# Kernel optimization log

Hardware: AMD Instinct MI355X
Metric: run time of the kernel (lower is better)

Reference implementation:

```python
import jax, jax.numpy as jnp
import numpy as np
import math

N_EMBED = 1024
N_HEAD = 16
HS = N_EMBED // N_HEAD

def setup_inputs() -> dict:
    key = jax.random.key(0)
    ks = jax.random.split(key, 5)
    s = 1.0 / math.sqrt(N_EMBED)
    x = jax.random.normal(ks[0], (2, 2048, N_EMBED), dtype=jnp.float32)
    W_qkv = jax.random.uniform(ks[1], (N_EMBED, 3 * N_EMBED), dtype=jnp.float32, minval=-s, maxval=s)
    b_qkv = jax.random.uniform(ks[2], (3 * N_EMBED,), dtype=jnp.float32, minval=-s, maxval=s)
    W_out = jax.random.uniform(ks[3], (N_EMBED, N_EMBED), dtype=jnp.float32, minval=-s, maxval=s)
    b_out = jax.random.uniform(ks[4], (N_EMBED,), dtype=jnp.float32, minval=-s, maxval=s)
    return {"x": x, "W_qkv": W_qkv, "b_qkv": b_qkv, "W_out": W_out, "b_out": b_out}

def reference(x, W_qkv, b_qkv, W_out, b_out):
    bs, seq_len, dim = x.shape
    qkv = x @ W_qkv + b_qkv                      # [b, s, 3*d]
    q, k, v = jnp.split(qkv, 3, axis=-1)
    def heads(t):
        return t.reshape(bs, seq_len, N_HEAD, HS).transpose(0, 2, 1, 3)  # [b, h, s, hs]
    q, k, v = heads(q), heads(k), heads(v)
    scale = 1.0 / math.sqrt(HS)
    attn = jnp.einsum('bhqd,bhkd->bhqk', q, k) * scale  # [b, h, s, s]
    causal = jnp.tril(jnp.ones((seq_len, seq_len), dtype=bool))
    attn = jnp.where(causal, attn, -jnp.inf)
    attn = jax.nn.softmax(attn, axis=-1)
    o = jnp.einsum('bhqk,bhkd->bhqd', attn, v)   # [b, h, s, hs]
    o = o.transpose(0, 2, 1, 3).reshape(bs, seq_len, dim)
    return o @ W_out + b_out
```

## Files before the change

### kernel.cpp

```cpp
#include <hip/hip_runtime.h>
#include <hip/hip_bf16.h>
#include <stdint.h>

typedef __attribute__((ext_vector_type(4))) float f32x4;
typedef __attribute__((ext_vector_type(8))) short s16x8;
typedef __attribute__((ext_vector_type(4))) short s16x4;

#define B_   2
#define S_   2048
#define D_   1024
#define H_   16
#define HS_  64
#define TOK  (B_*S_)
#define BH_  (B_*H_)

__device__ __forceinline__ short f2bf(float f){
  union { float f; uint32_t u; } v; v.f = f;
  uint32_t u = v.u;
  u += 0x7fffu + ((u >> 16) & 1u);
  return (short)(u >> 16);
}

__device__ __forceinline__ uint32_t cvt_pk_bf16(float lo, float hi){
  uint32_t r;
  asm("v_cvt_pk_bf16_f32 %0, %1, %2" : "=v"(r) : "v"(lo), "v"(hi));
  return r;
}

__device__ __forceinline__ void gload_lds16(const void* g, void* l){
  __builtin_amdgcn_global_load_lds((const __attribute__((address_space(1))) void*)g,
                                   (__attribute__((address_space(3))) void*)l, 16, 0, 0);
}

__global__ void k_cvt(const float* __restrict__ src, short* __restrict__ dst, int n4){
  int i = blockIdx.x * blockDim.x + threadIdx.x;
  if (i < n4){
    float4 v = reinterpret_cast<const float4*>(src)[i];
    s16x4 o;
    o.x = f2bf(v.x); o.y = f2bf(v.y); o.z = f2bf(v.z); o.w = f2bf(v.w);
    reinterpret_cast<s16x4*>(dst)[i] = o;
  }
}

__global__ void k_tconv(const float* __restrict__ src, short* __restrict__ dst, int K, int N){
  __shared__ short tile[32][33];
  const int n0 = blockIdx.x * 32, k0 = blockIdx.y * 32;
  const int c = threadIdx.x & 31, r8 = threadIdx.x >> 5;
  #pragma unroll
  for (int j = 0; j < 4; j++){
    int k = r8 + j * 8;
    tile[c][k] = f2bf(src[(size_t)(k0 + k) * N + n0 + c]);
  }
  __syncthreads();
  #pragma unroll
  for (int j = 0; j < 4; j++){
    int nl = r8 + j * 8;
    dst[(size_t)(n0 + nl) * K + k0 + c] = tile[nl][c];
  }
}

__global__ __launch_bounds__(256, 2) void k_gemm_qkv(
    const short* __restrict__ A, const short* __restrict__ Bt,
    const float* __restrict__ bias, short* __restrict__ Qb)
{
  __shared__ short Al[128 * 32];
  __shared__ short Bl[128 * 32];
  const int tid = threadIdx.x;
  const int lane = tid & 63, wave = tid >> 6;
  const int m0 = blockIdx.x * 128, n0 = blockIdx.y * 128;
  const int wm = (wave >> 1) * 64, wn = (wave & 1) * 64;
  const int c = lane & 15, g = lane >> 4;

  f32x4 acc[4][4];
  #pragma unroll
  for (int i = 0; i < 4; i++)
    #pragma unroll
    for (int j = 0; j < 4; j++) acc[i][j] = (f32x4){0.f, 0.f, 0.f, 0.f};

  const short* Asrc = A + (size_t)m0 * 1024;
  const short* Bsrc = Bt + (size_t)n0 * 1024;

  for (int kt = 0; kt < 1024; kt += 32){
    __syncthreads();
    #pragma unroll
    for (int j = 0; j < 2; j++){
      int gc = (wave * 2 + j) * 64 + lane;
      int row = gc >> 2, c8 = gc & 3;
      gload_lds16(Asrc + (size_t)row * 1024 + kt + c8 * 8, Al + (size_t)(wave * 2 + j) * 512);
      gload_lds16(Bsrc + (size_t)row * 1024 + kt + c8 * 8, Bl + (size_t)(wave * 2 + j) * 512);
    }
    __syncthreads();

    s16x8 af[4], bq[4];
    #pragma unroll
    for (int t = 0; t < 4; t++){
      af[t] = *(const s16x8*)&Al[(wm + t * 16 + c) * 32 + g * 8];
      bq[t] = *(const s16x8*)&Bl[(wn + t * 16 + c) * 32 + g * 8];
    }
    #pragma unroll
    for (int mt = 0; mt < 4; mt++)
      #pragma unroll
      for (int nt = 0; nt < 4; nt++)
        acc[mt][nt] = __builtin_amdgcn_mfma_f32_16x16x32_bf16(af[mt], bq[nt], acc[mt][nt], 0, 0, 0);
  }

  const size_t QSZ = (size_t)BH_ * S_ * HS_;
  #pragma unroll
  for (int mt = 0; mt < 4; mt++){
    #pragma unroll
    for (int nt = 0; nt < 4; nt++){
      int n = n0 + wn + nt * 16 + c;
      float bv = bias[n];
      int sel = n >> 10, hn = (n >> 6) & 15, d = n & 63;
      #pragma unroll
      for (int r = 0; r < 4; r++){
        int token = m0 + wm + mt * 16 + g * 4 + r;
        int b = token >> 11, s = token & 2047;
        float v = acc[mt][nt][r] + bv;
        Qb[(size_t)sel * QSZ + ((size_t)(b * H_ + hn) * S_ + s) * HS_ + d] = f2bf(v);
      }
    }
  }
}

__global__ __launch_bounds__(256, 2) void k_gemm_o(
    const short* __restrict__ A, const short* __restrict__ Bt,
    const float* __restrict__ bias, float* __restrict__ O)
{
  __shared__ short Al[64 * 32];
  __shared__ short Bl[128 * 32];
  const int tid = threadIdx.x;
  const int lane = tid & 63, wave = tid >> 6;
  const int m0 = blockIdx.x * 64, n0 = blockIdx.y * 128;
  const int wn = wave * 32;
  const int c = lane & 15, g = lane >> 4;

  f32x4 acc[4][2];
  #pragma unroll
  for (int i = 0; i < 4; i++)
    #pragma unroll
    for (int j = 0; j < 2; j++) acc[i][j] = (f32x4){0.f, 0.f, 0.f, 0.f};

  const short* Asrc = A + (size_t)m0 * 1024;
  const short* Bsrc = Bt + (size_t)n0 * 1024;

  for (int kt = 0; kt < 1024; kt += 32){
    __syncthreads();
    {
      int gc = wave * 64 + lane;
      int row = gc >> 2, c8 = gc & 3;
      gload_lds16(Asrc + (size_t)row * 1024 + kt + c8 * 8, Al + (size_t)wave * 512);
    }
    #pragma unroll
    for (int j = 0; j < 2; j++){
      int gc = (wave * 2 + j) * 64 + lane;
      int row = gc >> 2, c8 = gc & 3;
      gload_lds16(Bsrc + (size_t)row * 1024 + kt + c8 * 8, Bl + (size_t)(wave * 2 + j) * 512);
    }
    __syncthreads();

    s16x8 af[4], bq[2];
    #pragma unroll
    for (int t = 0; t < 4; t++)
      af[t] = *(const s16x8*)&Al[(t * 16 + c) * 32 + g * 8];
    #pragma unroll
    for (int n = 0; n < 2; n++)
      bq[n] = *(const s16x8*)&Bl[(wn + n * 16 + c) * 32 + g * 8];
    #pragma unroll
    for (int mt = 0; mt < 4; mt++)
      #pragma unroll
      for (int n = 0; n < 2; n++)
        acc[mt][n] = __builtin_amdgcn_mfma_f32_16x16x32_bf16(af[mt], bq[n], acc[mt][n], 0, 0, 0);
  }

  #pragma unroll
  for (int mt = 0; mt < 4; mt++){
    #pragma unroll
    for (int n = 0; n < 2; n++){
      int nn = n0 + wn + n * 16 + c;
      float bv = bias[nn];
      #pragma unroll
      for (int r = 0; r < 4; r++){
        int token = m0 + mt * 16 + g * 4 + r;
        O[(size_t)token * 1024 + nn] = acc[mt][n][r] + bv;
      }
    }
  }
}

__global__ void k_vtrans(const short* __restrict__ Vg, short* __restrict__ Vt){
  __shared__ short t[64 * 80];
  const int bh = blockIdx.y;
  const int s0 = blockIdx.x * 64;
  const int tid = threadIdx.x;
  const int r = tid >> 3, c8 = (tid & 7) * 8;
  #pragma unroll
  for (int p = 0; p < 2; p++){
    int ss = r + p * 32;
    s16x8 v = *(const s16x8*)&Vg[((size_t)bh * S_ + s0 + ss) * HS_ + c8];
    #pragma unroll
    for (int i = 0; i < 8; i++) t[(c8 + i) * 80 + ss] = v[i];
  }
  __syncthreads();
  #pragma unroll
  for (int p = 0; p < 2; p++){
    int d = r + p * 32;
    s16x8 v = *(const s16x8*)&t[d * 80 + c8];
    *(s16x8*)&Vt[((size_t)bh * HS_ + d) * S_ + s0 + c8] = v;
  }
}

__global__ __launch_bounds__(256, 3) void k_attn(
    const short* __restrict__ Qg, const short* __restrict__ Kg,
    const short* __restrict__ Vt, short* __restrict__ Og)
{
  __shared__ short Kl[2][64 * 64];
  __shared__ short Vl[2][64 * 64];
  __shared__ short Pl[4][32 * 64];

  const int tid = threadIdx.x, lane = tid & 63, wave = tid >> 6;
  const int c = lane & 15, g = lane >> 4;
  const int c7 = c & 7;

  const int p = blockIdx.x;
  const int qt = (p < 256) ? (15 - (p >> 5)) : ((p - 256) >> 5);
  const int bh = p & 31;
  const int q0 = qt * 128;
  const int q0w = q0 + wave * 32;
  const int nkt = 2 * qt + 2;
  const size_t basebh = (size_t)bh * S_ * HS_;
  const short* Kb  = Kg + basebh;
  const short* Vtb = Vt + (size_t)bh * HS_ * S_;

  s16x8 qb[2][2];
  #pragma unroll
  for (int rt = 0; rt < 2; rt++)
    #pragma unroll
    for (int h = 0; h < 2; h++)
      qb[rt][h] = *(const s16x8*)&Qg[basebh + (size_t)(q0w + rt * 16 + c) * HS_ + h * 32 + g * 8];

  f32x4 o_acc[2][4];
  #pragma unroll
  for (int rt = 0; rt < 2; rt++)
    #pragma unroll
    for (int nt = 0; nt < 4; nt++) o_acc[rt][nt] = (f32x4){0.f, 0.f, 0.f, 0.f};
  float m_[2] = {-3e38f, -3e38f}, l_[2] = {0.f, 0.f};

  short* Pw = &Pl[wave][0];
  const float SC = 0.125f * 1.44269504f;

  const int srow = tid >> 3;
  const int schk = tid & 7;
  const int swc  = ((schk ^ (srow & 7)) * 8);
  const int ldsoff0 = wave * 512;

  auto STAGE = [&](int buf, int kt){
    const int k0 = kt * 64;
    #pragma unroll
    for (int i = 0; i < 2; i++){
      gload_lds16(Kb + (size_t)(k0 + srow + 32 * i) * HS_ + swc, &Kl[buf][i * 2048 + ldsoff0]);
      gload_lds16(Vtb + (size_t)(srow + 32 * i) * S_ + k0 + swc, &Vl[buf][i * 2048 + ldsoff0]);
    }
  };

  auto COMPUTE = [&](int buf, int kt){
    const int k0 = kt * 64;
    const short* KB = &Kl[buf][0];
    const short* VB = &Vl[buf][0];

    s16x8 ka[4][2];
    #pragma unroll
    for (int kf = 0; kf < 4; kf++)
      #pragma unroll
      for (int h = 0; h < 2; h++)
        ka[kf][h] = *(const s16x8*)&KB[(kf * 16 + c) * 64 + ((h * 4 + g) ^ c7) * 8];

    #pragma unroll
    for (int rt = 0; rt < 2; rt++){
      const int qlo = q0w + rt * 16;
      if (k0 > qlo + 15) continue;

      f32x4 st[4];
      #pragma unroll
      for (int kf = 0; kf < 4; kf++){
        f32x4 a = (f32x4){0.f, 0.f, 0.f, 0.f};
        a = __builtin_amdgcn_mfma_f32_16x16x32_bf16(ka[kf][0], qb[rt][0], a, 0, 0, 0);
        a = __builtin_amdgcn_mfma_f32_16x16x32_bf16(ka[kf][1], qb[rt][1], a, 0, 0, 0);
        st[kf] = a;
      }

      const bool edge = (k0 + 63 > qlo);
      float sc[16];
      float tmax = -3e38f;
      #pragma unroll
      for (int kf = 0; kf < 4; kf++)
        #pragma unroll
        for (int r = 0; r < 4; r++){
          float v = st[kf][r];
          if (edge && (k0 + kf * 16 + g * 4 + r > qlo + c)) v = -3e38f;
          sc[kf * 4 + r] = v;
          tmax = fmaxf(tmax, v);
        }
      tmax = fmaxf(tmax, __shfl_xor(tmax, 16));
      tmax = fmaxf(tmax, __shfl_xor(tmax, 32));

      if (!__all(tmax <= m_[rt])){
        float mnew = fmaxf(m_[rt], tmax);
        float fe = exp2f((m_[rt] - mnew) * SC);
        m_[rt] = mnew;
        l_[rt] *= fe;
        float feq0 = __shfl(fe, g * 4 + 0), feq1 = __shfl(fe, g * 4 + 1);
        float feq2 = __shfl(fe, g * 4 + 2), feq3 = __shfl(fe, g * 4 + 3);
        #pragma unroll
        for (int nt = 0; nt < 4; nt++){
          f32x4 t = o_acc[rt][nt];
          t[0] *= feq0; t[1] *= feq1; t[2] *= feq2; t[3] *= feq3;
          o_acc[rt][nt] = t;
        }
      }

      const float nmsc = -m_[rt] * SC;
      float rs = 0.f;
      const int prow = rt * 16 + c;
      #pragma unroll
      for (int kf = 0; kf < 4; kf++){
        float p0 = exp2f(fmaf(sc[kf * 4 + 0], SC, nmsc));
        float p1 = exp2f(fmaf(sc[kf * 4 + 1], SC, nmsc));
        float p2 = exp2f(fmaf(sc[kf * 4 + 2], SC, nmsc));
        float p3 = exp2f(fmaf(sc[kf * 4 + 3], SC, nmsc));
        rs += (p0 + p1) + (p2 + p3);
        uint2 pk;
        pk.x = cvt_pk_bf16(p0, p1);
        pk.y = cvt_pk_bf16(p2, p3);
        *(uint2*)&Pw[prow * 64 + ((2 * kf + (g >> 1)) ^ c7) * 8 + (g & 1) * 4] = pk;
      }
      rs += __shfl_xor(rs, 16);
      rs += __shfl_xor(rs, 32);
      l_[rt] += rs;
    }

    s16x8 vb[4][2];
    #pragma unroll
    for (int nt = 0; nt < 4; nt++)
      #pragma unroll
      for (int ks = 0; ks < 2; ks++)
        vb[nt][ks] = *(const s16x8*)&VB[(nt * 16 + c) * 64 + ((ks * 4 + g) ^ c7) * 8];

    #pragma unroll
    for (int rt = 0; rt < 2; rt++){
      if (k0 > q0w + rt * 16 + 15) continue;
      #pragma unroll
      for (int ks = 0; ks < 2; ks++){
        s16x8 pa = *(const s16x8*)&Pw[(rt * 16 + c) * 64 + ((ks * 4 + g) ^ c7) * 8];
        #pragma unroll
        for (int nt = 0; nt < 4; nt++)
          o_acc[rt][nt] = __builtin_amdgcn_mfma_f32_16x16x32_bf16(pa, vb[nt][ks], o_acc[rt][nt], 0, 0, 0);
      }
    }
  };

  STAGE(0, 0);
  __syncthreads();
  int cur = 0;
  for (int t = 0; t < nkt; t++){
    if (t + 1 < nkt) STAGE(cur ^ 1, t + 1);
    COMPUTE(cur, t);
    __syncthreads();
    cur ^= 1;
  }

  const int h = bh & 15, b = bh >> 4;
  #pragma unroll
  for (int rt = 0; rt < 2; rt++){
    float linv = 1.0f / l_[rt];
    float lr0 = __shfl(linv, g * 4 + 0), lr1 = __shfl(linv, g * 4 + 1);
    float lr2 = __shfl(linv, g * 4 + 2), lr3 = __shfl(linv, g * 4 + 3);
    #pragma unroll
    for (int nt = 0; nt < 4; nt++){
      int q = q0w + rt * 16 + g * 4;
      size_t base = (size_t)(b * S_ + q) * D_ + h * HS_ + nt * 16 + c;
      Og[base]            = f2bf(o_acc[rt][nt][0] * lr0);
      Og[base + D_]       = f2bf(o_acc[rt][nt][1] * lr1);
      Og[base + 2 * D_]   = f2bf(o_acc[rt][nt][2] * lr2);
      Og[base + 3 * D_]   = f2bf(o_acc[rt][nt][3] * lr3);
    }
  }
}

extern "C" void kernel_launch(void* const* d_in, const int* in_sizes, int n_in,
                              void* d_out, int out_size, void* d_ws, size_t ws_size,
                              hipStream_t stream)
{
  const float* x    = (const float*)d_in[0];
  const float* Wqkv = (const float*)d_in[1];
  const float* bqkv = (const float*)d_in[2];
  const float* Wout = (const float*)d_in[3];
  const float* bout = (const float*)d_in[4];

  char* ws = (char*)d_ws;
  short* xb     = (short*)(ws);
  short* Wqkv_t = (short*)(ws + 8388608);
  short* Wout_t = (short*)(ws + 14680064);
  short* Qg     = (short*)(ws + 16777216);
  short* Kg     = Qg + 4194304;
  short* Vg     = Qg + 8388608;
  short* Vt     = (short*)(ws + 41943040);
  short* Otok   = xb;

  k_cvt<<<4096, 256, 0, stream>>>(x, xb, TOK * D_ / 4);
  k_tconv<<<dim3(96, 32), 256, 0, stream>>>(Wqkv, Wqkv_t, 1024, 3072);
  k_tconv<<<dim3(32, 32), 256, 0, stream>>>(Wout, Wout_t, 1024, 1024);
  k_gemm_qkv<<<dim3(32, 24), 256, 0, stream>>>(xb, Wqkv_t, bqkv, Qg);
  k_vtrans<<<dim3(32, 32), 256, 0, stream>>>(Vg, Vt);
  k_attn<<<dim3(512), 256, 0, stream>>>(Qg, Kg, Vt, Otok);
  k_gemm_o<<<dim3(64, 8), 256, 0, stream>>>(Otok, Wout_t, bout, (float*)d_out);
}
```

Measured before the change: 221.9 us.

## Halve attention query tile to 64 rows, double grid, single barrier per step

Each attention block now handles 64 query rows, 16 per wave, instead of 128, so the grid doubles to 1024 blocks. Tile ordering is reshuffled to balance the causal workload, and launch bounds rise to allow 4 blocks per CU. The two barriers per K/V step become one explicit vmcnt wait plus s_barrier, and setprio is wrapped around the MFMA sections. Each K/V tile is now reused by half as many queries, so loads from global memory and LDS roughly double per query, in exchange for more parallelism and occupancy.

```diff
diff --git a/kernel.cpp b/kernel.cpp
--- a/kernel.cpp
+++ b/kernel.cpp
@@ -210,41 +210,39 @@
   }
 }
 
-__global__ __launch_bounds__(256, 3) void k_attn(
+__global__ __launch_bounds__(256, 4) void k_attn(
     const short* __restrict__ Qg, const short* __restrict__ Kg,
     const short* __restrict__ Vt, short* __restrict__ Og)
 {
   __shared__ short Kl[2][64 * 64];
   __shared__ short Vl[2][64 * 64];
-  __shared__ short Pl[4][32 * 64];
+  __shared__ short Pl[4][16 * 64];
 
   const int tid = threadIdx.x, lane = tid & 63, wave = tid >> 6;
   const int c = lane & 15, g = lane >> 4;
   const int c7 = c & 7;
 
   const int p = blockIdx.x;
-  const int qt = (p < 256) ? (15 - (p >> 5)) : ((p - 256) >> 5);
-  const int bh = p & 31;
-  const int q0 = qt * 128;
-  const int q0w = q0 + wave * 32;
-  const int nkt = 2 * qt + 2;
+  const int j = p >> 5, bh = p & 31;
+  const int grp = j >> 3;
+  const int qt = (grp == 0 || grp == 2) ? (31 - j) : ((grp == 1) ? (j + 8) : (j - 24));
+  const int q0 = qt * 64;
+  const int q0w = q0 + wave * 16;
+  const int nkt = qt + 1;
   const size_t basebh = (size_t)bh * S_ * HS_;
   const short* Kb  = Kg + basebh;
   const short* Vtb = Vt + (size_t)bh * HS_ * S_;
 
-  s16x8 qb[2][2];
-  #pragma unroll
-  for (int rt = 0; rt < 2; rt++)
-    #pragma unroll
-    for (int h = 0; h < 2; h++)
-      qb[rt][h] = *(const s16x8*)&Qg[basebh + (size_t)(q0w + rt * 16 + c) * HS_ + h * 32 + g * 8];
-
-  f32x4 o_acc[2][4];
-  #pragma unroll
-  for (int rt = 0; rt < 2; rt++)
-    #pragma unroll
-    for (int nt = 0; nt < 4; nt++) o_acc[rt][nt] = (f32x4){0.f, 0.f, 0.f, 0.f};
-  float m_[2] = {-3e38f, -3e38f}, l_[2] = {0.f, 0.f};
+  s16x8 qb0, qb1;
+  {
+    const short* qp = Qg + basebh + (size_t)(q0w + c) * HS_ + g * 8;
+    qb0 = *(const s16x8*)qp;
+    qb1 = *(const s16x8*)(qp + 32);
+  }
+  f32x4 o_acc[4];
+  #pragma unroll
+  for (int nt = 0; nt < 4; nt++) o_acc[nt] = (f32x4){0.f, 0.f, 0.f, 0.f};
+  float m_ = -3e38f, l_ = 0.f;
 
   short* Pw = &Pl[wave][0];
   const float SC = 0.125f * 1.44269504f;
@@ -275,69 +273,64 @@
       for (int h = 0; h < 2; h++)
         ka[kf][h] = *(const s16x8*)&KB[(kf * 16 + c) * 64 + ((h * 4 + g) ^ c7) * 8];
 
-    #pragma unroll
-    for (int rt = 0; rt < 2; rt++){
-      const int qlo = q0w + rt * 16;
-      if (k0 > qlo + 15) continue;
-
-      f32x4 st[4];
-      #pragma unroll
-      for (int kf = 0; kf < 4; kf++){
-        f32x4 a = (f32x4){0.f, 0.f, 0.f, 0.f};
-        a = __builtin_amdgcn_mfma_f32_16x16x32_bf16(ka[kf][0], qb[rt][0], a, 0, 0, 0);
-        a = __builtin_amdgcn_mfma_f32_16x16x32_bf16(ka[kf][1], qb[rt][1], a, 0, 0, 0);
-        st[kf] = a;
+    f32x4 st[4];
+    __builtin_amdgcn_s_setprio(1);
+    #pragma unroll
+    for (int kf = 0; kf < 4; kf++){
+      f32x4 a = (f32x4){0.f, 0.f, 0.f, 0.f};
+      a = __builtin_amdgcn_mfma_f32_16x16x32_bf16(ka[kf][0], qb0, a, 0, 0, 0);
+      a = __builtin_amdgcn_mfma_f32_16x16x32_bf16(ka[kf][1], qb1, a, 0, 0, 0);
+      st[kf] = a;
+    }
+    __builtin_amdgcn_s_setprio(0);
+
+    const bool edge = (k0 + 63 > q0w);
+    float sc[16];
+    float tmax = -3e38f;
+    #pragma unroll
+    for (int kf = 0; kf < 4; kf++)
+      #pragma unroll
+      for (int r = 0; r < 4; r++){
+        float v = st[kf][r];
+        if (edge && (k0 + kf * 16 + g * 4 + r > q0w + c)) v = -3e38f;
+        sc[kf * 4 + r] = v;
+        tmax = fmaxf(tmax, v);
       }
-
-      const bool edge = (k0 + 63 > qlo);
-      float sc[16];
-      float tmax = -3e38f;
-      #pragma unroll
-      for (int kf = 0; kf < 4; kf++)
-        #pragma unroll
-        for (int r = 0; r < 4; r++){
-          float v = st[kf][r];
-          if (edge && (k0 + kf * 16 + g * 4 + r > qlo + c)) v = -3e38f;
-          sc[kf * 4 + r] = v;
-          tmax = fmaxf(tmax, v);
-        }
-      tmax = fmaxf(tmax, __shfl_xor(tmax, 16));
-      tmax = fmaxf(tmax, __shfl_xor(tmax, 32));
-
-      if (!__all(tmax <= m_[rt])){
-        float mnew = fmaxf(m_[rt], tmax);
-        float fe = exp2f((m_[rt] - mnew) * SC);
-        m_[rt] = mnew;
-        l_[rt] *= fe;
-        float feq0 = __shfl(fe, g * 4 + 0), feq1 = __shfl(fe, g * 4 + 1);
-        float feq2 = __shfl(fe, g * 4 + 2), feq3 = __shfl(fe, g * 4 + 3);
-        #pragma unroll
-        for (int nt = 0; nt < 4; nt++){
-          f32x4 t = o_acc[rt][nt];
-          t[0] *= feq0; t[1] *= feq1; t[2] *= feq2; t[3] *= feq3;
-          o_acc[rt][nt] = t;
-        }
+    tmax = fmaxf(tmax, __shfl_xor(tmax, 16));
+    tmax = fmaxf(tmax, __shfl_xor(tmax, 32));
+
+    if (!__all(tmax <= m_)){
+      float mnew = fmaxf(m_, tmax);
+      float fe = exp2f((m_ - mnew) * SC);
+      m_ = mnew;
+      l_ *= fe;
+      float feq0 = __shfl(fe, g * 4 + 0), feq1 = __shfl(fe, g * 4 + 1);
+      float feq2 = __shfl(fe, g * 4 + 2), feq3 = __shfl(fe, g * 4 + 3);
+      #pragma unroll
+      for (int nt = 0; nt < 4; nt++){
+        f32x4 t = o_acc[nt];
+        t[0] *= feq0; t[1] *= feq1; t[2] *= feq2; t[3] *= feq3;
+        o_acc[nt] = t;
       }
-
-      const float nmsc = -m_[rt] * SC;
-      float rs = 0.f;
-      const int prow = rt * 16 + c;
-      #pragma unroll
-      for (int kf = 0; kf < 4; kf++){
-        float p0 = exp2f(fmaf(sc[kf * 4 + 0], SC, nmsc));
-        float p1 = exp2f(fmaf(sc[kf * 4 + 1], SC, nmsc));
-        float p2 = exp2f(fmaf(sc[kf * 4 + 2], SC, nmsc));
-        float p3 = exp2f(fmaf(sc[kf * 4 + 3], SC, nmsc));
-        rs += (p0 + p1) + (p2 + p3);
-        uint2 pk;
-        pk.x = cvt_pk_bf16(p0, p1);
-        pk.y = cvt_pk_bf16(p2, p3);
-        *(uint2*)&Pw[prow * 64 + ((2 * kf + (g >> 1)) ^ c7) * 8 + (g & 1) * 4] = pk;
-      }
-      rs += __shfl_xor(rs, 16);
-      rs += __shfl_xor(rs, 32);
-      l_[rt] += rs;
-    }
+    }
+
+    const float nmsc = -m_ * SC;
+    float rs = 0.f;
+    #pragma unroll
+    for (int kf = 0; kf < 4; kf++){
+      float p0 = exp2f(fmaf(sc[kf * 4 + 0], SC, nmsc));
+      float p1 = exp2f(fmaf(sc[kf * 4 + 1], SC, nmsc));
+      float p2 = exp2f(fmaf(sc[kf * 4 + 2], SC, nmsc));
+      float p3 = exp2f(fmaf(sc[kf * 4 + 3], SC, nmsc));
+      rs += (p0 + p1) + (p2 + p3);
+      uint2 pk;
+      pk.x = cvt_pk_bf16(p0, p1);
+      pk.y = cvt_pk_bf16(p2, p3);
+      *(uint2*)&Pw[c * 64 + ((2 * kf + (g >> 1)) ^ c7) * 8 + (g & 1) * 4] = pk;
+    }
+    rs += __shfl_xor(rs, 16);
+    rs += __shfl_xor(rs, 32);
+    l_ += rs;
 
     s16x8 vb[4][2];
     #pragma unroll
@@ -346,44 +339,40 @@
       for (int ks = 0; ks < 2; ks++)
         vb[nt][ks] = *(const s16x8*)&VB[(nt * 16 + c) * 64 + ((ks * 4 + g) ^ c7) * 8];
 
-    #pragma unroll
-    for (int rt = 0; rt < 2; rt++){
-      if (k0 > q0w + rt * 16 + 15) continue;
-      #pragma unroll
-      for (int ks = 0; ks < 2; ks++){
-        s16x8 pa = *(const s16x8*)&Pw[(rt * 16 + c) * 64 + ((ks * 4 + g) ^ c7) * 8];
-        #pragma unroll
-        for (int nt = 0; nt < 4; nt++)
-          o_acc[rt][nt] = __builtin_amdgcn_mfma_f32_16x16x32_bf16(pa, vb[nt][ks], o_acc[rt][nt], 0, 0, 0);
-      }
-    }
+    __builtin_amdgcn_s_setprio(1);
+    #pragma unroll
+    for (int ks = 0; ks < 2; ks++){
+      s16x8 pa = *(const s16x8*)&Pw[c * 64 + ((ks * 4 + g) ^ c7) * 8];
+      #pragma unroll
+      for (int nt = 0; nt < 4; nt++)
+        o_acc[nt] = __builtin_amdgcn_mfma_f32_16x16x32_bf16(pa, vb[nt][ks], o_acc[nt], 0, 0, 0);
+    }
+    __builtin_amdgcn_s_setprio(0);
   };
 
   STAGE(0, 0);
-  __syncthreads();
   int cur = 0;
   for (int t = 0; t < nkt; t++){
+    asm volatile("s_waitcnt vmcnt(0)" ::: "memory");
+    __builtin_amdgcn_s_barrier();
+    asm volatile("" ::: "memory");
     if (t + 1 < nkt) STAGE(cur ^ 1, t + 1);
     COMPUTE(cur, t);
-    __syncthreads();
     cur ^= 1;
   }
 
   const int h = bh & 15, b = bh >> 4;
-  #pragma unroll
-  for (int rt = 0; rt < 2; rt++){
-    float linv = 1.0f / l_[rt];
-    float lr0 = __shfl(linv, g * 4 + 0), lr1 = __shfl(linv, g * 4 + 1);
-    float lr2 = __shfl(linv, g * 4 + 2), lr3 = __shfl(linv, g * 4 + 3);
-    #pragma unroll
-    for (int nt = 0; nt < 4; nt++){
-      int q = q0w + rt * 16 + g * 4;
-      size_t base = (size_t)(b * S_ + q) * D_ + h * HS_ + nt * 16 + c;
-      Og[base]            = f2bf(o_acc[rt][nt][0] * lr0);
-      Og[base + D_]       = f2bf(o_acc[rt][nt][1] * lr1);
-      Og[base + 2 * D_]   = f2bf(o_acc[rt][nt][2] * lr2);
-      Og[base + 3 * D_]   = f2bf(o_acc[rt][nt][3] * lr3);
-    }
+  float linv = 1.0f / l_;
+  float lr0 = __shfl(linv, g * 4 + 0), lr1 = __shfl(linv, g * 4 + 1);
+  float lr2 = __shfl(linv, g * 4 + 2), lr3 = __shfl(linv, g * 4 + 3);
+  #pragma unroll
+  for (int nt = 0; nt < 4; nt++){
+    int q = q0w + g * 4;
+    size_t base = (size_t)(b * S_ + q) * D_ + h * HS_ + nt * 16 + c;
+    Og[base]          = f2bf(o_acc[nt][0] * lr0);
+    Og[base + D_]     = f2bf(o_acc[nt][1] * lr1);
+    Og[base + 2 * D_] = f2bf(o_acc[nt][2] * lr2);
+    Og[base + 3 * D_] = f2bf(o_acc[nt][3] * lr3);
   }
 }
 
@@ -412,6 +401,6 @@
   k_tconv<<<dim3(32, 32), 256, 0, stream>>>(Wout, Wout_t, 1024, 1024);
   k_gemm_qkv<<<dim3(32, 24), 256, 0, stream>>>(xb, Wqkv_t, bqkv, Qg);
   k_vtrans<<<dim3(32, 32), 256, 0, stream>>>(Vg, Vt);
-  k_attn<<<dim3(512), 256, 0, stream>>>(Qg, Kg, Vt, Otok);
+  k_attn<<<dim3(1024), 256, 0, stream>>>(Qg, Kg, Vt, Otok);
   k_gemm_o<<<dim3(64, 8), 256, 0, stream>>>(Otok, Wout_t, bout, (float*)d_out);
 }
```

Measured after the change: 195.7 us. -11.8%, faster.
